# Performance work log

Measured on AMD Instinct MI355X. Metric: run time of the kernel, lower is better.

The kernel has to match this reference:

```python
import jax, jax.numpy as jnp
import numpy as np

D_MODEL = 2048
D_INNER = 2 * D_MODEL      # expand=2
D_STATE = 16
D_CONV = 4
DT_RANK = D_MODEL // 16    # ceil(2048/16)=128
BATCH, SEQLEN = 2, 1024


def setup_inputs() -> dict:
    key = jax.random.key(0)
    ks = jax.random.split(key, 10)
    s = 0.02
    inp = {
        "hidden_states": jax.random.normal(ks[0], (BATCH, SEQLEN, D_MODEL), jnp.float32),
        "in_proj_w": jax.random.normal(ks[1], (2 * D_INNER, D_MODEL), jnp.float32) * s,
        "conv_w": jax.random.normal(ks[2], (D_INNER, D_CONV), jnp.float32) * s,
        "conv_b": jax.random.normal(ks[3], (D_INNER,), jnp.float32) * s,
        "x_proj_w": jax.random.normal(ks[4], (DT_RANK + 2 * D_STATE, D_INNER), jnp.float32) * s,
        "dt_proj_w": jax.random.normal(ks[5], (D_INNER, DT_RANK), jnp.float32) * s,
        "dt_proj_b": jax.random.normal(ks[6], (D_INNER,), jnp.float32) * 0.1,
        "A_log": jnp.log(jnp.tile(jnp.arange(1, D_STATE + 1, dtype=jnp.float32), (D_INNER, 1))),
        "D": jnp.ones((D_INNER,), jnp.float32),
        "out_proj_w": jax.random.normal(ks[7], (D_MODEL, D_INNER), jnp.float32) * s,
    }
    return inp


def _mamba_forward(hidden_states, in_proj_w, conv_w, conv_b, x_proj_w,
                   dt_proj_w, dt_proj_b, A_log, D, out_proj_w):
    B, L, _ = hidden_states.shape
    # input projection -> x, z  (each [B, L, D_INNER])
    xz = jnp.einsum('bld,ed->ble', hidden_states, in_proj_w)
    x, z = jnp.split(xz, 2, axis=-1)
    # causal depthwise conv1d (kernel D_CONV) + SiLU
    x_pad = jnp.pad(x, ((0, 0), (D_CONV - 1, 0), (0, 0)))
    windows = jnp.stack([x_pad[:, k:k + L, :] for k in range(D_CONV)], axis=-1)  # [B,L,D,K]
    x_conv = jnp.einsum('bldk,dk->bld', windows, conv_w) + conv_b
    x_act = jax.nn.silu(x_conv)
    # data-dependent SSM parameters
    x_dbl = jnp.einsum('bld,ed->ble', x_act, x_proj_w)
    dt, Bc, Cc = jnp.split(x_dbl, [DT_RANK, DT_RANK + D_STATE], axis=-1)
    dt = jax.nn.softplus(jnp.einsum('blr,dr->bld', dt, dt_proj_w) + dt_proj_b)  # [B,L,D_INNER]
    A = -jnp.exp(A_log)  # [D_INNER, D_STATE]

    # selective scan over time (carry h: [B, D_INNER, D_STATE])
    def step(h, inp):
        x_t, dt_t, B_t, C_t = inp  # [B,D],[B,D],[B,N],[B,N]
        dA = jnp.exp(dt_t[:, :, None] * A[None])          # [B,D,N]
        dBx = dt_t[:, :, None] * B_t[:, None, :] * x_t[:, :, None]
        h = h * dA + dBx
        y = jnp.einsum('bdn,bn->bd', h, C_t)
        return h, y

    xs = (x_act.transpose(1, 0, 2), dt.transpose(1, 0, 2),
          Bc.transpose(1, 0, 2), Cc.transpose(1, 0, 2))
    h0 = jnp.zeros((B, D_INNER, D_STATE), x_act.dtype)
    _, ys = jax.lax.scan(step, h0, xs)          # [L,B,D_INNER]
    y = ys.transpose(1, 0, 2) + x_act * D       # skip connection D*x
    y = y * jax.nn.silu(z)                      # gating
    return jnp.einsum('bld,md->blm', y, out_proj_w)


def reference(hidden_states, in_proj_w, conv_w, conv_b, x_proj_w,
              dt_proj_w, dt_proj_b, A_log, D, out_proj_w):
    return _mamba_forward(hidden_states, in_proj_w, conv_w, conv_b, x_proj_w,
                          dt_proj_w, dt_proj_b, A_log, D, out_proj_w)
```

## Files before the change

kernel.cpp:

```cpp
#include <hip/hip_runtime.h>
#include <cstdint>
#include <cstddef>

#define D_MODEL 2048
#define D_INNER 4096
#define D_IN2   8192
#define D_STATE 16
#define D_CONVK 4
#define DT_RANK 128
#define BATCH   2
#define SEQLEN  1024
#define BL      (BATCH*SEQLEN)
#define XDBL_N  (DT_RANK + 2*D_STATE)
#define XPW_NPAD 256
#define XPROJ_SPLITS 8
#define OUT_SPLITS 2

#define NCHUNK  16
#define LCHUNK  (SEQLEN/NCHUNK)
#define CHW     (BATCH*D_INNER*D_STATE)

#define NB_HID   2048
#define NB_IPW   8192
#define NB_XPW   320
#define NB_XPWZ  192
#define NB_DTW   256
#define NB_OPW   4096
#define NB_XDBLZ 320

typedef short  s8v  __attribute__((ext_vector_type(8)));
typedef float  f4v  __attribute__((ext_vector_type(4)));

__device__ __forceinline__ float softplus_f(float v) {
    return (v > 20.f) ? v : log1pf(__expf(v));
}
__device__ __forceinline__ float silu_f(float v) {
    return v / (1.f + __expf(-v));
}
__device__ __forceinline__ float exp2_f(float x) {
    float r; asm("v_exp_f32 %0, %1" : "=v"(r) : "v"(x)); return r;
}
__device__ __forceinline__ float bf2f(short s) {
    return __uint_as_float(((uint32_t)(uint16_t)s) << 16);
}
__device__ __forceinline__ uint16_t f2bf(float f) {
    uint32_t u = __float_as_uint(f);
    return (uint16_t)((u + 0x7FFFu + ((u >> 16) & 1u)) >> 16);
}
__device__ __forceinline__ uint32_t packbf(float lo, float hi) {
    return ((uint32_t)f2bf(hi) << 16) | (uint32_t)f2bf(lo);
}
__device__ __forceinline__ float quad_sum(float p) {
    p += __int_as_float(__builtin_amdgcn_update_dpp(
            0, __float_as_int(p), 0xB1, 0xF, 0xF, true));
    p += __int_as_float(__builtin_amdgcn_update_dpp(
            0, __float_as_int(p), 0x4E, 0xF, 0xF, true));
    return p;
}

#define GLD16(gp, lp)                                                          \
    __builtin_amdgcn_global_load_lds(                                          \
        (const __attribute__((address_space(1))) void*)(gp),                   \
        (__attribute__((address_space(3))) void*)(lp), 16, 0, 0)

__global__ __launch_bounds__(256)
void k_cast_all(const float* __restrict__ s0, uint32_t* __restrict__ d0,
                const float* __restrict__ s1, uint32_t* __restrict__ d1,
                const float* __restrict__ s2, uint32_t* __restrict__ d2,
                const float* __restrict__ s3, uint32_t* __restrict__ d3,
                const float* __restrict__ s4, uint32_t* __restrict__ d4,
                uint32_t* __restrict__ z0, uint32_t* __restrict__ z1)
{
    int blk = blockIdx.x;
    const float* src = nullptr; uint32_t* dst; int base; int zero = 0;
    if      (blk < NB_HID) { src = s0; dst = d0; base = blk; }
    else if ((blk -= NB_HID)  < NB_IPW)  { src = s1; dst = d1; base = blk; }
    else if ((blk -= NB_IPW)  < NB_XPW)  { src = s2; dst = d2; base = blk; }
    else if ((blk -= NB_XPW)  < NB_XPWZ) { dst = z0; base = blk; zero = 1; }
    else if ((blk -= NB_XPWZ) < NB_DTW)  { src = s3; dst = d3; base = blk; }
    else if ((blk -= NB_DTW)  < NB_OPW)  { src = s4; dst = d4; base = blk; }
    else                                 { dst = z1; base = blk - NB_OPW; zero = 1; }
    const int i = base * 256 + threadIdx.x;
    if (zero) { ((uint4*)dst)[i] = make_uint4(0u, 0u, 0u, 0u); return; }
    const float4 a = ((const float4*)src)[i * 2];
    const float4 b = ((const float4*)src)[i * 2 + 1];
    uint4 o;
    o.x = packbf(a.x, a.y); o.y = packbf(a.z, a.w);
    o.z = packbf(b.x, b.y); o.w = packbf(b.z, b.w);
    ((uint4*)dst)[i] = o;
}

template<int EPI>
__device__ __forceinline__
void gemm_body(const short* __restrict__ A, int lda,
               const short* __restrict__ W, int ldw,
               void* __restrict__ Cv, int ldc, int M, int kchunk)
{
    constexpr int SMEM_BYTES = (EPI == 2) ? 34816 : (EPI == 0) ? 33792 : 32768;
    __shared__ __align__(16) char smem[SMEM_BYTES];
    short* sA = (short*)smem;
    short* sW = (short*)(smem + 16384);

    const int tid = threadIdx.x;
    const int w   = tid >> 6;
    const int L   = tid & 63;
    const int bm  = blockIdx.y * 128;
    const int bn  = blockIdx.x * 128;
    const int k0  = blockIdx.z * kchunk;

    const int rsub = L >> 3;
    const int c8   = (((L & 7) - rsub) & 7) * 8;
    const short* Ag[4]; const short* Wg[4];
#pragma unroll
    for (int j = 0; j < 4; j++) {
        Ag[j] = A + (size_t)(bm + w * 32 + j * 8 + rsub) * lda + c8 + k0;
        Wg[j] = W + (size_t)(bn + w * 32 + j * 8 + rsub) * ldw + c8 + k0;
    }

    const int wm = (w >> 1) * 64;
    const int wn = (w & 1) * 64;
    const int cl = L & 15;
    const int qd = L >> 4;

    f4v acc[4][4];
#pragma unroll
    for (int i = 0; i < 4; i++)
#pragma unroll
        for (int j = 0; j < 4; j++) acc[i][j] = (f4v){0.f, 0.f, 0.f, 0.f};

    for (int k = 0; k < kchunk; k += 64) {
#pragma unroll
        for (int j = 0; j < 4; j++)
            GLD16(Ag[j] + k, &sA[(w * 32 + j * 8) * 64]);
#pragma unroll
        for (int j = 0; j < 4; j++)
            GLD16(Wg[j] + k, &sW[(w * 32 + j * 8) * 64]);
        __syncthreads();
#pragma unroll
        for (int kk = 0; kk < 2; kk++) {
            const int sl = ((kk * 4 + qd + cl) & 7) * 8;
            s8v a[4], b[4];
#pragma unroll
            for (int mt = 0; mt < 4; mt++)
                a[mt] = *(const s8v*)&sA[(wm + mt * 16 + cl) * 64 + sl];
#pragma unroll
            for (int nt = 0; nt < 4; nt++)
                b[nt] = *(const s8v*)&sW[(wn + nt * 16 + cl) * 64 + sl];
#pragma unroll
            for (int mt = 0; mt < 4; mt++)
#pragma unroll
                for (int nt = 0; nt < 4; nt++)
                    acc[mt][nt] = __builtin_amdgcn_mfma_f32_16x16x32_bf16(
                        a[mt], b[nt], acc[mt][nt], 0, 0, 0);
        }
        __syncthreads();
    }

    if constexpr (EPI == 2) {
        ushort (*sC)[136] = (ushort(*)[136])smem;
        short* Cs = (short*)Cv;
#pragma unroll
        for (int mt = 0; mt < 4; mt++)
#pragma unroll
            for (int nt = 0; nt < 4; nt++)
#pragma unroll
                for (int r = 0; r < 4; r++)
                    sC[wm + mt * 16 + qd * 4 + r][wn + nt * 16 + cl] =
                        (ushort)f2bf(acc[mt][nt][r]);
        __syncthreads();
#pragma unroll
        for (int it = 0; it < 8; it++) {
            const int idx = it * 256 + tid;
            const int row = idx >> 4;
            const int c8s = (idx & 15) * 8;
            *(uint4*)&Cs[(size_t)(bm + row) * ldc + bn + c8s] =
                *(const uint4*)&sC[row][c8s];
        }
    } else if constexpr (EPI == 0) {
        float (*sC)[132] = (float(*)[132])smem;
        float* Cf = (float*)Cv + (size_t)blockIdx.z * M * ldc;
#pragma unroll
        for (int half = 0; half < 2; half++) {
            __syncthreads();
            if (wm == half * 64) {
#pragma unroll
                for (int mt = 0; mt < 4; mt++)
#pragma unroll
                    for (int nt = 0; nt < 4; nt++)
#pragma unroll
                        for (int r = 0; r < 4; r++)
                            sC[mt * 16 + qd * 4 + r][wn + nt * 16 + cl] =
                                acc[mt][nt][r];
            }
            __syncthreads();
#pragma unroll
            for (int it = 0; it < 8; it++) {
                const int f4  = it * 256 + tid;
                const int row = f4 >> 5;
                const int c4  = (f4 & 31) * 4;
                const float4 v = *(const float4*)&sC[row][c4];
                *(float4*)&Cf[(size_t)(bm + half * 64 + row) * ldc + bn + c4] = v;
            }
        }
    } else {
        float* Cf = (float*)Cv;
#pragma unroll
        for (int mt = 0; mt < 4; mt++) {
            const int row0 = bm + wm + mt * 16 + qd * 4;
#pragma unroll
            for (int nt = 0; nt < 4; nt++) {
                const int col = bn + wn + nt * 16 + cl;
                if (col >= XDBL_N) continue;
#pragma unroll
                for (int r = 0; r < 4; r++)
                    atomicAdd(&Cf[(size_t)(row0 + r) * ldc + col], acc[mt][nt][r]);
            }
        }
    }
}

__global__ __launch_bounds__(256)
void k_gemm_inproj(const short* A, const short* W, short* C)
{ gemm_body<2>(A, D_MODEL, W, D_MODEL, C, D_IN2, BL, D_MODEL); }

__global__ __launch_bounds__(256)
void k_gemm_xproj(const short* A, const short* W, float* C)
{ gemm_body<3>(A, D_INNER, W, D_INNER, C, XDBL_N, BL, D_INNER / XPROJ_SPLITS); }

__global__ __launch_bounds__(256)
void k_gemm_outproj(const short* A, const short* W, float* C)
{ gemm_body<0>(A, D_INNER, W, D_INNER, C, D_MODEL, BL, D_INNER / OUT_SPLITS); }

__global__ __launch_bounds__(256)
void k_gemm_dt(const float* __restrict__ Af, const short* __restrict__ W,
               float* __restrict__ C)
{
    __shared__ __align__(16) char smem[65536];
    short* sA = (short*)smem;
    short* sW = (short*)(smem + 32768);

    const int tid = threadIdx.x;
    const int w   = tid >> 6;
    const int L   = tid & 63;
    const int bm  = blockIdx.y * 128;
    const int bn  = blockIdx.x * 128;

#pragma unroll
    for (int ci = 0; ci < 8; ci++) {
        const int c_lin = tid * 8 + ci;
        const int r = c_lin >> 4;
        const int c = c_lin & 15;
        const float* src = Af + (size_t)(bm + r) * XDBL_N + c * 8;
        const float4 u = *(const float4*)src;
        const float4 v = *(const float4*)(src + 4);
        const int half = c >> 3, cc = c & 7;
        const int slot = (cc + r) & 7;
        uint4 o;
        o.x = packbf(u.x, u.y); o.y = packbf(u.z, u.w);
        o.z = packbf(v.x, v.y); o.w = packbf(v.z, v.w);
        *(uint4*)&sA[half * 8192 + r * 64 + slot * 8] = o;
    }
    const int rsub = L >> 3;
    const int c8   = (((L & 7) - rsub) & 7) * 8;
#pragma unroll
    for (int half = 0; half < 2; half++)
#pragma unroll
        for (int j = 0; j < 4; j++)
            GLD16(W + (size_t)(bn + w * 32 + j * 8 + rsub) * DT_RANK + half * 64 + c8,
                  &sW[half * 8192 + (w * 32 + j * 8) * 64]);
    __syncthreads();

    const int wm = (w >> 1) * 64;
    const int wn = (w & 1) * 64;
    const int cl = L & 15;
    const int qd = L >> 4;

    f4v acc[4][4];
#pragma unroll
    for (int i = 0; i < 4; i++)
#pragma unroll
        for (int j = 0; j < 4; j++) acc[i][j] = (f4v){0.f, 0.f, 0.f, 0.f};

#pragma unroll
    for (int ks = 0; ks < 4; ks++) {
        const int half = ks >> 1;
        const int sl = (((ks & 1) * 4 + qd + cl) & 7) * 8;
        s8v a[4], b[4];
#pragma unroll
        for (int mt = 0; mt < 4; mt++)
            a[mt] = *(const s8v*)&sA[half * 8192 + (wm + mt * 16 + cl) * 64 + sl];
#pragma unroll
        for (int nt = 0; nt < 4; nt++)
            b[nt] = *(const s8v*)&sW[half * 8192 + (wn + nt * 16 + cl) * 64 + sl];
#pragma unroll
        for (int mt = 0; mt < 4; mt++)
#pragma unroll
            for (int nt = 0; nt < 4; nt++)
                acc[mt][nt] = __builtin_amdgcn_mfma_f32_16x16x32_bf16(
                    a[mt], b[nt], acc[mt][nt], 0, 0, 0);
    }

    __syncthreads();
    float (*sC)[132] = (float(*)[132])smem;
#pragma unroll
    for (int half = 0; half < 2; half++) {
        __syncthreads();
        if (wm == half * 64) {
#pragma unroll
            for (int mt = 0; mt < 4; mt++)
#pragma unroll
                for (int nt = 0; nt < 4; nt++)
#pragma unroll
                    for (int r = 0; r < 4; r++)
                        sC[mt * 16 + qd * 4 + r][wn + nt * 16 + cl] =
                            acc[mt][nt][r];
        }
        __syncthreads();
#pragma unroll
        for (int it = 0; it < 8; it++) {
            const int f4  = it * 256 + tid;
            const int row = f4 >> 5;
            const int c4  = (f4 & 31) * 4;
            const float4 v = *(const float4*)&sC[row][c4];
            *(float4*)&C[(size_t)(bm + half * 64 + row) * D_INNER + bn + c4] = v;
        }
    }
}

__global__ __launch_bounds__(256)
void k_reduce_out(const float* __restrict__ P, float* __restrict__ out)
{
    const int i = blockIdx.x * 256 + threadIdx.x;
    const float4 a = ((const float4*)P)[i];
    const float4 b = ((const float4*)(P + (size_t)BL * D_MODEL))[i];
    ((float4*)out)[i] = make_float4(a.x + b.x, a.y + b.y, a.z + b.z, a.w + b.w);
}

__global__ __launch_bounds__(256)
void k_conv(const short* __restrict__ xz_bf, const float* __restrict__ cw,
            const float* __restrict__ cb, short* __restrict__ x_bf)
{
    const int idx = blockIdx.x * 256 + threadIdx.x;
    const int d  = idx & (D_INNER - 1);
    const int bl = idx >> 12;
    const int l  = bl & (SEQLEN - 1);
    const int b  = bl >> 10;
    const short* xb = xz_bf + (size_t)b * SEQLEN * D_IN2 + d;
    float acc = cb[d];
#pragma unroll
    for (int k = 0; k < D_CONVK; k++) {
        const int ll = l + k - (D_CONVK - 1);
        if (ll >= 0) acc = fmaf(bf2f(xb[(size_t)ll * D_IN2]), cw[d * D_CONVK + k], acc);
    }
    x_bf[idx] = (short)f2bf(silu_f(acc));
}

__global__ __launch_bounds__(256)
void k_scan_p1(const short* __restrict__ x_bf, const float* __restrict__ dtr,
               const float* __restrict__ dtb, const float* __restrict__ xdbl,
               const float* __restrict__ A_log,
               float* __restrict__ h_end, float* __restrict__ Pprod)
{
    const int c   = blockIdx.y;
    const int ch0 = blockIdx.x * 64;
    const int b   = ch0 >> 12;
    const int d0  = ch0 & (D_INNER - 1);
    const int tid = threadIdx.x;
    const int g   = tid >> 2;
    const int q   = tid & 3;
    const int d   = d0 + g;

    const float LOG2E = 1.44269504f;
    const float4 Al = *(const float4*)&A_log[(d << 4) + (q << 2)];
    float An[4] = {-__expf(Al.x) * LOG2E, -__expf(Al.y) * LOG2E,
                   -__expf(Al.z) * LOG2E, -__expf(Al.w) * LOG2E};
    float h[4]  = {0.f, 0.f, 0.f, 0.f};
    float Pp[4] = {1.f, 1.f, 1.f, 1.f};

    __shared__ float s_x [16][68];
    __shared__ float s_dt[16][68];
    __shared__ float s_B [16][20];

    const int lt  = tid >> 4;
    const int ld4 = (tid & 15) * 4;
    const float4 bb = *(const float4*)&dtb[d0 + ld4];

    for (int sub = 0; sub < LCHUNK / 16; sub++) {
        const int l0 = c * LCHUNK + sub * 16;
        const size_t bl = (size_t)(b * SEQLEN + l0 + lt);
        __syncthreads();
        {
            const short4 sx = *(const short4*)&x_bf[bl * D_INNER + d0 + ld4];
            const float4 dv = *(const float4*)&dtr[bl * D_INNER + d0 + ld4];
            *(float4*)&s_x [lt][ld4] =
                make_float4(bf2f(sx.x), bf2f(sx.y), bf2f(sx.z), bf2f(sx.w));
            *(float4*)&s_dt[lt][ld4] = make_float4(
                softplus_f(dv.x + bb.x), softplus_f(dv.y + bb.y),
                softplus_f(dv.z + bb.z), softplus_f(dv.w + bb.w));
            if (tid < 64) {
                const int t2 = tid >> 2, k = (tid & 3) * 4;
                const size_t bl2 = (size_t)(b * SEQLEN + l0 + t2);
                *(float4*)&s_B[t2][k] =
                    *(const float4*)&xdbl[bl2 * XDBL_N + DT_RANK + k];
            }
        }
        __syncthreads();
#pragma unroll
        for (int t = 0; t < 16; t++) {
            const float xv  = s_x [t][g];
            const float dtv = s_dt[t][g];
            const float4 Bq = *(const float4*)&s_B[t][q * 4];
            const float Bv[4] = {Bq.x, Bq.y, Bq.z, Bq.w};
            const float dtx = dtv * xv;
#pragma unroll
            for (int j = 0; j < 4; j++) {
                const float dA = exp2_f(dtv * An[j]);
                h[j]  = fmaf(h[j], dA, dtx * Bv[j]);
                Pp[j] *= dA;
            }
        }
    }
    const size_t i0 = (size_t)c * CHW + (((size_t)(b * D_INNER + d)) << 4) + (q << 2);
    *(float4*)&h_end[i0] = make_float4(h[0], h[1], h[2], h[3]);
    *(float4*)&Pprod[i0] = make_float4(Pp[0], Pp[1], Pp[2], Pp[3]);
}

__global__ __launch_bounds__(256)
void k_scan_p3(const short* __restrict__ x_bf, short* __restrict__ y_bf,
               const float* __restrict__ dtr, const float* __restrict__ dtb,
               const float* __restrict__ xdbl,
               const short* __restrict__ xz_bf, const float* __restrict__ A_log,
               const float* __restrict__ Dvec,
               const float* __restrict__ h_end, const float* __restrict__ Pbuf)
{
    const int c   = blockIdx.y;
    const int ch0 = blockIdx.x * 64;
    const int b   = ch0 >> 12;
    const int d0  = ch0 & (D_INNER - 1);
    const int tid = threadIdx.x;
    const int g   = tid >> 2;
    const int q   = tid & 3;
    const int d   = d0 + g;

    const float LOG2E = 1.44269504f;
    const float4 Al = *(const float4*)&A_log[(d << 4) + (q << 2)];
    float An[4] = {-__expf(Al.x) * LOG2E, -__expf(Al.y) * LOG2E,
                   -__expf(Al.z) * LOG2E, -__expf(Al.w) * LOG2E};
    const float Dd = Dvec[d];

    float h[4] = {0.f, 0.f, 0.f, 0.f};
    const size_t base = (((size_t)(b * D_INNER + d)) << 4) + (q << 2);
    {
        int j = 0;
        for (; j + 4 <= c; j += 4) {
            float4 he[4], Pq[4];
#pragma unroll
            for (int u = 0; u < 4; u++) {
                he[u] = *(const float4*)&h_end[(size_t)(j + u) * CHW + base];
                Pq[u] = *(const float4*)&Pbuf [(size_t)(j + u) * CHW + base];
            }
#pragma unroll
            for (int u = 0; u < 4; u++) {
                h[0] = fmaf(Pq[u].x, h[0], he[u].x);
                h[1] = fmaf(Pq[u].y, h[1], he[u].y);
                h[2] = fmaf(Pq[u].z, h[2], he[u].z);
                h[3] = fmaf(Pq[u].w, h[3], he[u].w);
            }
        }
        for (; j < c; j++) {
            const float4 he = *(const float4*)&h_end[(size_t)j * CHW + base];
            const float4 Pq = *(const float4*)&Pbuf [(size_t)j * CHW + base];
            h[0] = fmaf(Pq.x, h[0], he.x);
            h[1] = fmaf(Pq.y, h[1], he.y);
            h[2] = fmaf(Pq.z, h[2], he.z);
            h[3] = fmaf(Pq.w, h[3], he.w);
        }
    }

    __shared__ float s_x [16][68];
    __shared__ float s_dt[16][68];
    __shared__ float s_z [16][68];
    __shared__ float s_B [16][20];
    __shared__ float s_C [16][20];

    const int lt  = tid >> 4;
    const int ld4 = (tid & 15) * 4;
    const float4 bb = *(const float4*)&dtb[d0 + ld4];

    for (int sub = 0; sub < LCHUNK / 16; sub++) {
        const int l0 = c * LCHUNK + sub * 16;
        const size_t bl = (size_t)(b * SEQLEN + l0 + lt);
        __syncthreads();
        {
            const short4 sx = *(const short4*)&x_bf[bl * D_INNER + d0 + ld4];
            const float4 dv = *(const float4*)&dtr[bl * D_INNER + d0 + ld4];
            const short4 zv = *(const short4*)&xz_bf[bl * D_IN2 + D_INNER + d0 + ld4];
            *(float4*)&s_x [lt][ld4] =
                make_float4(bf2f(sx.x), bf2f(sx.y), bf2f(sx.z), bf2f(sx.w));
            *(float4*)&s_dt[lt][ld4] = make_float4(
                softplus_f(dv.x + bb.x), softplus_f(dv.y + bb.y),
                softplus_f(dv.z + bb.z), softplus_f(dv.w + bb.w));
            *(float4*)&s_z [lt][ld4] = make_float4(
                silu_f(bf2f(zv.x)), silu_f(bf2f(zv.y)),
                silu_f(bf2f(zv.z)), silu_f(bf2f(zv.w)));
            if (tid < 128) {
                const int t2 = (tid & 63) >> 2, k = (tid & 3) * 4;
                const size_t bl2 = (size_t)(b * SEQLEN + l0 + t2);
                const int off = (tid < 64) ? 0 : D_STATE;
                const float4 v =
                    *(const float4*)&xdbl[bl2 * XDBL_N + DT_RANK + off + k];
                if (tid < 64) *(float4*)&s_B[t2][k] = v;
                else          *(float4*)&s_C[t2][k] = v;
            }
        }
        __syncthreads();
        const size_t orow = (size_t)(b * SEQLEN + l0);
#pragma unroll
        for (int t = 0; t < 16; t++) {
            const float xv  = s_x [t][g];
            const float dtv = s_dt[t][g];
            const float4 Bq = *(const float4*)&s_B[t][q * 4];
            const float4 Cq = *(const float4*)&s_C[t][q * 4];
            const float Bv[4] = {Bq.x, Bq.y, Bq.z, Bq.w};
            const float Cv[4] = {Cq.x, Cq.y, Cq.z, Cq.w};
            const float dtx = dtv * xv;
            float p = 0.f;
#pragma unroll
            for (int j = 0; j < 4; j++) {
                const float dA = exp2_f(dtv * An[j]);
                h[j] = fmaf(h[j], dA, dtx * Bv[j]);
                p = fmaf(h[j], Cv[j], p);
            }
            p = quad_sum(p);
            if (q == 0) {
                const float yv = fmaf(xv, Dd, p) * s_z[t][g];
                y_bf[(orow + t) * D_INNER + d] = (short)f2bf(yv);
            }
        }
    }
}

extern "C" void kernel_launch(void* const* d_in, const int* in_sizes, int n_in,
                              void* d_out, int out_size, void* d_ws, size_t ws_size,
                              hipStream_t stream)
{
    const float* hidden     = (const float*)d_in[0];
    const float* in_proj_w  = (const float*)d_in[1];
    const float* conv_w     = (const float*)d_in[2];
    const float* conv_b     = (const float*)d_in[3];
    const float* x_proj_w   = (const float*)d_in[4];
    const float* dt_proj_w  = (const float*)d_in[5];
    const float* dt_proj_b  = (const float*)d_in[6];
    const float* A_log      = (const float*)d_in[7];
    const float* Dvec       = (const float*)d_in[8];
    const float* out_proj_w = (const float*)d_in[9];
    float* out = (float*)d_out;

    const size_t MB = 1ull << 20;
    char* ws = (char*)d_ws;
    short* xz_bf   = (short*)(ws);
    short* x_bf    = (short*)(ws + 32 * MB);
    short* ipw_bf  = (short*)(ws + 48 * MB);
    short* y_bf    = (short*)(ws + 48 * MB);
    float* h_end   = (float*)(ws + 64 * MB);
    float* Pbuf    = (float*)(ws + 72 * MB);
    short* hid_bf  = (short*)(ws + 80 * MB);
    short* opw_bf  = (short*)(ws + 88 * MB);
    float* dt_raw  = (float*)(ws + 104 * MB);
    float* op_part = (float*)(ws + 104 * MB);
    short* xpw_bf  = (short*)(ws + 136 * MB);
    short* dtw_bf  = (short*)(ws + 138 * MB);
    float* xdbl_f  = (float*)(ws + 139 * MB);

    const dim3 blk(256);

    k_cast_all<<<dim3(NB_HID + NB_IPW + NB_XPW + NB_XPWZ + NB_DTW + NB_OPW + NB_XDBLZ),
                blk, 0, stream>>>(
        hidden, (uint32_t*)hid_bf, in_proj_w, (uint32_t*)ipw_bf,
        x_proj_w, (uint32_t*)xpw_bf, dt_proj_w, (uint32_t*)dtw_bf,
        out_proj_w, (uint32_t*)opw_bf,
        (uint32_t*)(xpw_bf + (size_t)XDBL_N * D_INNER),
        (uint32_t*)xdbl_f);

    k_gemm_inproj<<<dim3(D_IN2 / 128, BL / 128, 1), blk, 0, stream>>>(
        hid_bf, ipw_bf, xz_bf);

    k_conv<<<dim3((BL * D_INNER) / 256), blk, 0, stream>>>(
        xz_bf, conv_w, conv_b, x_bf);

    k_gemm_xproj<<<dim3(XPW_NPAD / 128, BL / 128, XPROJ_SPLITS), blk, 0, stream>>>(
        x_bf, xpw_bf, xdbl_f);

    k_gemm_dt<<<dim3(D_INNER / 128, BL / 128), blk, 0, stream>>>(
        xdbl_f, dtw_bf, dt_raw);

    k_scan_p1<<<dim3(BATCH * D_INNER / 64, NCHUNK - 1), blk, 0, stream>>>(
        x_bf, dt_raw, dt_proj_b, xdbl_f, A_log, h_end, Pbuf);
    k_scan_p3<<<dim3(BATCH * D_INNER / 64, NCHUNK), blk, 0, stream>>>(
        x_bf, y_bf, dt_raw, dt_proj_b, xdbl_f, xz_bf, A_log, Dvec, h_end, Pbuf);

    k_gemm_outproj<<<dim3(D_MODEL / 128, BL / 128, OUT_SPLITS), blk, 0, stream>>>(
        y_bf, opw_bf, op_part);
    k_reduce_out<<<dim3(BL * D_MODEL / 4 / 256), blk, 0, stream>>>(op_part, out);
}
```

Baseline: 451.8 us.

## Rewrite in_proj GEMM as 256x256 tile, 512-thread, double-buffered pipelined kernel

Replaces the generic 128x128 in_proj GEMM with a dedicated kernel that computes 256x256 tiles using 512 threads (8 waves). Global-to-LDS loads are double-buffered and split into K-halves, and explicit barriers, waitcnts, sched_barriers and setprio interleave the next tile's loads with the MFMA phases. This raises data reuse per LDS byte and hides global load latency. The cost is 128KB of LDS and 128 accumulators per thread, which limits occupancy. The grid shrinks to 32x8 blocks, which may underfill the CUs.

```diff
diff --git a/kernel.cpp b/kernel.cpp
--- a/kernel.cpp
+++ b/kernel.cpp
@@ -90,13 +90,169 @@
     ((uint4*)dst)[i] = o;
 }
 
+__global__ __launch_bounds__(512, 2)
+void k_gemm_inproj(const short* __restrict__ A, const short* __restrict__ W,
+                   short* __restrict__ C)
+{
+    constexpr int LDA = D_MODEL;
+    constexpr int LDC = D_IN2;
+    constexpr int NT  = D_MODEL / 64;
+
+    __shared__ __align__(16) short smem[65536];
+
+    const int tid = threadIdx.x;
+    const int w   = tid >> 6;
+    const int L   = tid & 63;
+    const int bm  = blockIdx.y * 256;
+    const int bn  = blockIdx.x * 256;
+
+    const int srow = tid >> 2;
+    const int g    = ((tid & 3) - (tid >> 3)) & 3;
+    const short* Ag0 = A + (size_t)(bm + srow) * LDA + g * 8;
+    const short* Ag1 = Ag0 + (size_t)128 * LDA;
+    const short* Wg0 = W + (size_t)(bn + srow) * LDA + g * 8;
+    const short* Wg1 = Wg0 + (size_t)128 * LDA;
+    const int wofs = w * 512;
+
+#define STG_A(t_, kh_) do {                                                    \
+        GLD16(Ag0 + (size_t)(t_) * 64 + (kh_) * 32,                            \
+              smem + (((t_) & 1) * 16384 + (kh_) * 8192 + wofs));              \
+        GLD16(Ag1 + (size_t)(t_) * 64 + (kh_) * 32,                            \
+              smem + (((t_) & 1) * 16384 + (kh_) * 8192 + 4096 + wofs));       \
+    } while (0)
+#define STG_B(t_, kh_) do {                                                    \
+        GLD16(Wg0 + (size_t)(t_) * 64 + (kh_) * 32,                            \
+              smem + (32768 + ((t_) & 1) * 16384 + (kh_) * 8192 + wofs));      \
+        GLD16(Wg1 + (size_t)(t_) * 64 + (kh_) * 32,                            \
+              smem + (32768 + ((t_) & 1) * 16384 + (kh_) * 8192 + 4096 + wofs));\
+    } while (0)
+
+    const int wm = w >> 2;
+    const int wn = w & 3;
+    const int cl = L & 15;
+    const int qd = L >> 4;
+    const int slot  = (qd + (cl >> 1)) & 3;
+    const int abase = (wm * 128 + cl) * 32 + slot * 8;
+    const int bbase = (wn * 64 + cl) * 32 + slot * 8;
+
+    f4v acc[8][4];
+#pragma unroll
+    for (int i = 0; i < 8; i++)
+#pragma unroll
+        for (int j = 0; j < 4; j++) acc[i][j] = (f4v){0.f, 0.f, 0.f, 0.f};
+
+#define LDS8(p) (*(const s8v*)(p))
+#define MF(m_, n_, aa_, bb_)                                                   \
+    acc[m_][n_] = __builtin_amdgcn_mfma_f32_16x16x32_bf16(                     \
+        aa_, bb_, acc[m_][n_], 0, 0, 0)
+#define MF16(m0_)                                                              \
+    MF(m0_ + 0, 0, a0, b0); MF(m0_ + 1, 0, a1, b0);                            \
+    MF(m0_ + 2, 0, a2, b0); MF(m0_ + 3, 0, a3, b0);                            \
+    MF(m0_ + 0, 1, a0, b1); MF(m0_ + 1, 1, a1, b1);                            \
+    MF(m0_ + 2, 1, a2, b1); MF(m0_ + 3, 1, a3, b1);                            \
+    MF(m0_ + 0, 2, a0, b2); MF(m0_ + 1, 2, a1, b2);                            \
+    MF(m0_ + 2, 2, a2, b2); MF(m0_ + 3, 2, a3, b2);                            \
+    MF(m0_ + 0, 3, a0, b3); MF(m0_ + 1, 3, a1, b3);                            \
+    MF(m0_ + 2, 3, a2, b3); MF(m0_ + 3, 3, a3, b3)
+#define PH_SYNC() do {                                                         \
+        __builtin_amdgcn_s_barrier();                                          \
+        asm volatile("s_waitcnt lgkmcnt(0)" ::: "memory");                     \
+        __builtin_amdgcn_sched_barrier(0);                                     \
+    } while (0)
+
+    STG_A(0, 0); STG_B(0, 0);
+    __builtin_amdgcn_sched_barrier(0);
+    STG_A(0, 1); STG_B(0, 1);
+    __builtin_amdgcn_sched_barrier(0);
+    STG_A(1, 0); STG_B(1, 0);
+    asm volatile("s_waitcnt vmcnt(4)" ::: "memory");
+    __builtin_amdgcn_s_barrier();
+
+#pragma unroll 2
+    for (int t = 0; t < NT; ++t) {
+        const short* pA = smem + (t & 1) * 16384;
+        const short* pB = smem + 32768 + (t & 1) * 16384;
+        s8v a0, a1, a2, a3, b0, b1, b2, b3;
+
+        a0 = LDS8(pA + abase);        a1 = LDS8(pA + abase + 512);
+        a2 = LDS8(pA + abase + 1024); a3 = LDS8(pA + abase + 1536);
+        b0 = LDS8(pB + bbase);        b1 = LDS8(pB + bbase + 512);
+        b2 = LDS8(pB + bbase + 1024); b3 = LDS8(pB + bbase + 1536);
+        if (t + 1 < NT) STG_A(t + 1, 1);
+        PH_SYNC();
+        __builtin_amdgcn_s_setprio(1);
+        MF16(0);
+        __builtin_amdgcn_s_setprio(0);
+        __builtin_amdgcn_s_barrier();
+
+        a0 = LDS8(pA + abase + 2048); a1 = LDS8(pA + abase + 2560);
+        a2 = LDS8(pA + abase + 3072); a3 = LDS8(pA + abase + 3584);
+        if (t + 1 < NT) STG_B(t + 1, 1);
+        PH_SYNC();
+        __builtin_amdgcn_s_setprio(1);
+        MF16(4);
+        __builtin_amdgcn_s_setprio(0);
+        __builtin_amdgcn_s_barrier();
+
+        a0 = LDS8(pA + 8192 + abase);        a1 = LDS8(pA + 8192 + abase + 512);
+        a2 = LDS8(pA + 8192 + abase + 1024); a3 = LDS8(pA + 8192 + abase + 1536);
+        b0 = LDS8(pB + 8192 + bbase);        b1 = LDS8(pB + 8192 + bbase + 512);
+        b2 = LDS8(pB + 8192 + bbase + 1024); b3 = LDS8(pB + 8192 + bbase + 1536);
+        if (t + 2 < NT) STG_A(t + 2, 0);
+        PH_SYNC();
+        __builtin_amdgcn_s_setprio(1);
+        MF16(0);
+        __builtin_amdgcn_s_setprio(0);
+        __builtin_amdgcn_s_barrier();
+
+        a0 = LDS8(pA + 8192 + abase + 2048); a1 = LDS8(pA + 8192 + abase + 2560);
+        a2 = LDS8(pA + 8192 + abase + 3072); a3 = LDS8(pA + 8192 + abase + 3584);
+        if (t + 2 < NT) STG_B(t + 2, 0);
+        PH_SYNC();
+        __builtin_amdgcn_s_setprio(1);
+        MF16(4);
+        __builtin_amdgcn_s_setprio(0);
+        if (t < NT - 2) asm volatile("s_waitcnt vmcnt(4)" ::: "memory");
+        else            asm volatile("s_waitcnt vmcnt(0)" ::: "memory");
+        __builtin_amdgcn_s_barrier();
+    }
+#undef MF16
+#undef MF
+#undef LDS8
+#undef STG_A
+#undef STG_B
+#undef PH_SYNC
+
+    {
+        ushort (*sC)[256] = (ushort(*)[256])smem;
+#pragma unroll
+        for (int mt = 0; mt < 8; mt++)
+#pragma unroll
+            for (int nt = 0; nt < 4; nt++)
+#pragma unroll
+                for (int r = 0; r < 4; r++)
+                    sC[wm * 128 + mt * 16 + qd * 4 + r][wn * 64 + nt * 16 + cl] =
+                        (ushort)f2bf(acc[mt][nt][r]);
+        asm volatile("s_waitcnt lgkmcnt(0)" ::: "memory");
+        __builtin_amdgcn_s_barrier();
+#pragma unroll
+        for (int it = 0; it < 16; it++) {
+            const int idx = it * 512 + tid;
+            const int row = idx >> 5;
+            const int c8s = (idx & 31) * 8;
+            *(uint4*)&C[(size_t)(bm + row) * LDC + bn + c8s] =
+                *(const uint4*)&sC[row][c8s];
+        }
+    }
+}
+
 template<int EPI>
 __device__ __forceinline__
 void gemm_body(const short* __restrict__ A, int lda,
                const short* __restrict__ W, int ldw,
                void* __restrict__ Cv, int ldc, int M, int kchunk)
 {
-    constexpr int SMEM_BYTES = (EPI == 2) ? 34816 : (EPI == 0) ? 33792 : 32768;
+    constexpr int SMEM_BYTES = (EPI == 0) ? 33792 : 32768;
     __shared__ __align__(16) char smem[SMEM_BYTES];
     short* sA = (short*)smem;
     short* sW = (short*)(smem + 16384);
@@ -156,27 +312,7 @@
         __syncthreads();
     }
 
-    if constexpr (EPI == 2) {
-        ushort (*sC)[136] = (ushort(*)[136])smem;
-        short* Cs = (short*)Cv;
-#pragma unroll
-        for (int mt = 0; mt < 4; mt++)
-#pragma unroll
-            for (int nt = 0; nt < 4; nt++)
-#pragma unroll
-                for (int r = 0; r < 4; r++)
-                    sC[wm + mt * 16 + qd * 4 + r][wn + nt * 16 + cl] =
-                        (ushort)f2bf(acc[mt][nt][r]);
-        __syncthreads();
-#pragma unroll
-        for (int it = 0; it < 8; it++) {
-            const int idx = it * 256 + tid;
-            const int row = idx >> 4;
-            const int c8s = (idx & 15) * 8;
-            *(uint4*)&Cs[(size_t)(bm + row) * ldc + bn + c8s] =
-                *(const uint4*)&sC[row][c8s];
-        }
-    } else if constexpr (EPI == 0) {
+    if constexpr (EPI == 0) {
         float (*sC)[132] = (float(*)[132])smem;
         float* Cf = (float*)Cv + (size_t)blockIdx.z * M * ldc;
 #pragma unroll
@@ -218,10 +354,6 @@
         }
     }
 }
-
-__global__ __launch_bounds__(256)
-void k_gemm_inproj(const short* A, const short* W, short* C)
-{ gemm_body<2>(A, D_MODEL, W, D_MODEL, C, D_IN2, BL, D_MODEL); }
 
 __global__ __launch_bounds__(256)
 void k_gemm_xproj(const short* A, const short* W, float* C)
@@ -582,7 +714,7 @@
         (uint32_t*)(xpw_bf + (size_t)XDBL_N * D_INNER),
         (uint32_t*)xdbl_f);
 
-    k_gemm_inproj<<<dim3(D_IN2 / 128, BL / 128, 1), blk, 0, stream>>>(
+    k_gemm_inproj<<<dim3(D_IN2 / 256, BL / 256), dim3(512), 0, stream>>>(
         hid_bf, ipw_bf, xz_bf);
 
     k_conv<<<dim3((BL * D_INNER) / 256), blk, 0, stream>>>(
```

After: 441.8 us. 1.02x faster.
